# Performance work log

Measured on AMD Instinct MI355X. Metric: run time of the kernel, lower is better.

## Reference

```python
import jax, jax.numpy as jnp
import numpy as np

C_M, C_Z, C = 256, 128, 32
N_SEQ, N_RES = 128, 256


def setup_inputs() -> dict:
    key = jax.random.key(0)
    ks = jax.random.split(key, 8)
    m = jax.random.normal(ks[0], (N_SEQ, N_RES, C_M), dtype=jnp.float32)
    gamma = jnp.ones((C_M,), dtype=jnp.float32)
    beta = jnp.zeros((C_M,), dtype=jnp.float32)
    s = 1.0 / np.sqrt(C_M)
    W1 = jax.random.normal(ks[1], (C_M, C), dtype=jnp.float32) * s
    b1 = jax.random.normal(ks[2], (C,), dtype=jnp.float32) * 0.01
    W2 = jax.random.normal(ks[3], (C_M, C), dtype=jnp.float32) * s
    b2 = jax.random.normal(ks[4], (C,), dtype=jnp.float32) * 0.01
    Wout = jax.random.normal(ks[5], (C * C, C_Z), dtype=jnp.float32) / np.sqrt(C * C)
    bout = jax.random.normal(ks[6], (C_Z,), dtype=jnp.float32) * 0.01
    return {"m": m, "gamma": gamma, "beta": beta, "W1": W1, "b1": b1,
            "W2": W2, "b2": b2, "Wout": Wout, "bout": bout}


def _layernorm(x, gamma, beta, eps=1e-5):
    mu = jnp.mean(x, axis=-1, keepdims=True)
    var = jnp.var(x, axis=-1, keepdims=True)
    return (x - mu) * jax.lax.rsqrt(var + eps) * gamma + beta


def reference(m, gamma, beta, W1, b1, W2, b2, Wout, bout):
    n_seq = m.shape[-3]
    mn = _layernorm(m, gamma, beta)              # (s, i, c_m)
    a = mn @ W1 + b1                              # (s, i, c)
    b = mn @ W2 + b2                              # (s, j, c)
    o = jnp.einsum('sic,sjk->ijck', a, b)        # (i, j, c, c)
    o = o.reshape(o.shape[0], o.shape[1], -1)    # (i, j, c*c)
    z = (o @ Wout + bout) / n_seq                # (i, j, c_z)
    return z
```

## Files before the change

kernel.cpp:

```cpp
#include <hip/hip_runtime.h>
#include <hip/hip_bf16.h>

typedef __attribute__((ext_vector_type(8))) short short8;
typedef __attribute__((ext_vector_type(4))) short short4v;
typedef __attribute__((ext_vector_type(4))) float f32x4;

#define WS_A   0
#define WS_B   (8192 * 128 * 2)
#define WS_WT  (2 * 8192 * 128 * 2)
#define WS_W12 (WS_WT + 128 * 1024 * 2)

static __device__ __forceinline__ short f2bf(float x) {
    __hip_bfloat16 h = __float2bfloat16(x);
    return *reinterpret_cast<short*>(&h);
}

typedef __attribute__((address_space(3))) unsigned int lds_u32;
typedef const __attribute__((address_space(1))) unsigned int glb_u32;
static __device__ __forceinline__ void stage16(const void* g, void* l) {
    __builtin_amdgcn_global_load_lds((glb_u32*)g, (lds_u32*)l, 16, 0, 0);
}

__global__ __launch_bounds__(256) void k_prep(const float* __restrict__ Wout,
                                              const float* __restrict__ W1,
                                              const float* __restrict__ W2,
                                              __hip_bfloat16* __restrict__ WoutT,
                                              __hip_bfloat16* __restrict__ W12bf) {
    int idx = blockIdx.x * 256 + threadIdx.x;
    if (blockIdx.x < 512) {
        int z = idx >> 10, ck = idx & 1023;
        WoutT[idx] = __float2bfloat16(Wout[ck * 128 + z]);
    } else {
        idx -= 512 * 256;
        int c = idx >> 8, d = idx & 255;
        W12bf[idx] = __float2bfloat16(c < 32 ? W1[d * 32 + c] : W2[d * 32 + (c - 32)]);
    }
}

__global__ __launch_bounds__(256) void k_lnproj(const float* __restrict__ mm,
                                                const float* __restrict__ gamma,
                                                const float* __restrict__ beta,
                                                const float* __restrict__ b1,
                                                const float* __restrict__ b2,
                                                const __hip_bfloat16* __restrict__ W12bf,
                                                __hip_bfloat16* __restrict__ Ap,
                                                __hip_bfloat16* __restrict__ Bp) {
    __shared__ char sMN[4][8192];
    __shared__ char sW[32768];
    const int t    = threadIdx.x;
    const int lane = t & 63;
    const int wid  = t >> 6;
    const int gw   = blockIdx.x * 4 + wid;
    const int i_   = gw & 255;
    const int sb   = (gw >> 8) * 16;

    #pragma unroll
    for (int it = 0; it < 8; it++) {
        const int idx = it * 256 + t;
        const int row = idx >> 5;
        const int L   = (idx & 31) * 16;
        *(short8*)(sW + row * 512 + (L ^ ((row & 7) << 4))) =
            *(const short8*)((const short*)W12bf + idx * 8);
    }

    float4 g4  = *(const float4*)&gamma[lane * 4];
    float4 be4 = *(const float4*)&beta[lane * 4];
    char* my = sMN[wid];

    #pragma unroll
    for (int rr = 0; rr < 16; rr++) {
        float4 x = *(const float4*)&mm[((size_t)(sb + rr) * 256 + i_) * 256 + lane * 4];
        float s  = x.x + x.y + x.z + x.w;
        float ss = x.x * x.x + x.y * x.y + x.z * x.z + x.w * x.w;
        #pragma unroll
        for (int off = 32; off; off >>= 1) {
            s  += __shfl_xor(s, off);
            ss += __shfl_xor(ss, off);
        }
        float mu  = s * (1.f / 256.f);
        float var = ss * (1.f / 256.f) - mu * mu;
        float rs  = rsqrtf(var + 1e-5f);
        short4v v;
        v.x = f2bf((x.x - mu) * rs * g4.x + be4.x);
        v.y = f2bf((x.y - mu) * rs * g4.y + be4.y);
        v.z = f2bf((x.z - mu) * rs * g4.z + be4.z);
        v.w = f2bf((x.w - mu) * rs * g4.w + be4.w);
        *(short4v*)(my + rr * 512 + ((lane * 8) ^ ((rr & 7) << 4))) = v;
    }
    __syncthreads();

    const int g = lane >> 4, r16 = lane & 15;

    f32x4 acc[4];
    #pragma unroll
    for (int nf = 0; nf < 4; nf++) {
        int col = nf * 16 + r16;
        float bv = (col < 32) ? b1[col] : b2[col - 32];
        acc[nf] = (f32x4){bv, bv, bv, bv};
    }
    #pragma unroll
    for (int ks = 0; ks < 8; ks++) {
        const int L = ks * 64 + g * 16;
        short8 af = *(const short8*)(my + r16 * 512 + (L ^ ((r16 & 7) << 4)));
        #pragma unroll
        for (int nf = 0; nf < 4; nf++) {
            short8 bfv = *(const short8*)(sW + (nf * 16 + r16) * 512 + (L ^ ((r16 & 7) << 4)));
            acc[nf] = __builtin_amdgcn_mfma_f32_16x16x32_bf16(af, bfv, acc[nf], 0, 0, 0);
        }
    }
    #pragma unroll
    for (int nf = 0; nf < 4; nf++) {
        int col = nf * 16 + r16;
        short* Out = (short*)((col < 32) ? Ap : Bp);
        int cr = col & 31;
        short4v v;
        v.x = f2bf(acc[nf][0]); v.y = f2bf(acc[nf][1]);
        v.z = f2bf(acc[nf][2]); v.w = f2bf(acc[nf][3]);
        *(short4v*)&Out[(i_ * 32 + cr) * 128 + sb + g * 4] = v;
    }
}

extern __shared__ char lds[];

__global__ __launch_bounds__(512, 1) void k_gemm6(const __hip_bfloat16* __restrict__ Apb,
                                                  const __hip_bfloat16* __restrict__ Bpb,
                                                  const __hip_bfloat16* __restrict__ WoutT,
                                                  const float* __restrict__ bout,
                                                  float* __restrict__ out) {
    const int t = threadIdx.x, lane = t & 63, wid = t >> 6;
    const int g = lane >> 4, r16 = lane & 15;
    const int wr = wid >> 2, wc = wid & 3;
    const int bid = (blockIdx.x & 7) * 128 + (blockIdx.x >> 3);
    const int bi = bid >> 5, bj = bid & 31;

    const short* gA = (const short*)Apb + (size_t)bi * 256 * 128;
    const short* gB = (const short*)Bpb + (size_t)bj * 256 * 128;

    const int srow8 = lane >> 3;
    const int sgran = (lane & 7) ^ srow8;
    #pragma unroll
    for (int kh = 0; kh < 2; kh++) {
        #pragma unroll
        for (int rd = 0; rd < 4; rd++) {
            const int row = rd * 64 + wid * 8 + srow8;
            stage16(gB + row * 128 + kh * 64 + sgran * 8,
                    lds + kh * 65536 + rd * 8192 + wid * 1024);
            stage16(gA + row * 128 + kh * 64 + sgran * 8,
                    lds + kh * 65536 + 32768 + rd * 8192 + wid * 1024);
        }
    }

    asm volatile("s_waitcnt vmcnt(8)" ::: "memory");
    __builtin_amdgcn_s_barrier();

    f32x4 acc[8][4];
    #pragma unroll
    for (int mf = 0; mf < 8; mf++)
        #pragma unroll
        for (int nf = 0; nf < 4; nf++)
            acc[mf][nf] = (f32x4){0.f, 0.f, 0.f, 0.f};

    #pragma unroll
    for (int kh = 0; kh < 2; kh++) {
        if (kh) {
            asm volatile("s_waitcnt vmcnt(0)" ::: "memory");
            __builtin_amdgcn_s_barrier();
        }
        const char* sBb = lds + kh * 65536;
        const char* sAb = lds + kh * 65536 + 32768;
        #pragma unroll
        for (int ksl = 0; ksl < 2; ksl++) {
            short8 af[8], bfv[4];
            #pragma unroll
            for (int mf = 0; mf < 8; mf++) {
                const int row = wr * 128 + mf * 16 + r16;
                af[mf] = *(const short8*)(sBb + row * 128 + (((ksl * 4 + g) ^ (row & 7)) << 4));
            }
            #pragma unroll
            for (int nf = 0; nf < 4; nf++) {
                const int row = wc * 64 + nf * 16 + r16;
                bfv[nf] = *(const short8*)(sAb + row * 128 + (((ksl * 4 + g) ^ (row & 7)) << 4));
            }
            __builtin_amdgcn_s_setprio(1);
            #pragma unroll
            for (int mf = 0; mf < 8; mf++)
                #pragma unroll
                for (int nf = 0; nf < 4; nf++)
                    acc[mf][nf] = __builtin_amdgcn_mfma_f32_16x16x32_bf16(af[mf], bfv[nf], acc[mf][nf], 0, 0, 0);
            __builtin_amdgcn_s_setprio(0);
        }
    }
    __builtin_amdgcn_s_barrier();

    const int z = wid * 16 + r16;
    const float bv = bout[z];
    f32x4 acc2[4];
    #pragma unroll
    for (int pf = 0; pf < 4; pf++) acc2[pf] = (f32x4){bv, bv, bv, bv};
    const short* wtz = (const short*)WoutT + z * 1024 + g * 8;

    short8 wA[4], wB[4];

    #define WLOAD(buf, h, grp)                                                           \
        {                                                                                \
            _Pragma("unroll")                                                            \
            for (int q = 0; q < 4; q++)                                                  \
                buf[q] = *(const short8*)&wtz[(h) * 512 + ((grp) * 4 + q) * 32];         \
        }

    #define WCOMP(buf, h, grp)                                                           \
        {                                                                                \
            const char* sPh = lds + (h) * 65536;                                         \
            __builtin_amdgcn_s_setprio(1);                                               \
            _Pragma("unroll")                                                            \
            for (int q = 0; q < 4; q++) {                                                \
                const int L = ((grp) * 4 + q) * 64 + g * 16;                             \
                _Pragma("unroll")                                                        \
                for (int pf = 0; pf < 4; pf++) {                                         \
                    const int row = pf * 16 + r16;                                       \
                    short8 pv = *(const short8*)(sPh + row * 1024 +                      \
                                                 (L ^ ((((L >> 7) ^ row) & 7) << 4)));   \
                    acc2[pf] = __builtin_amdgcn_mfma_f32_16x16x32_bf16(pv, buf[q], acc2[pf], 0, 0, 0); \
                }                                                                        \
            }                                                                            \
            __builtin_amdgcn_s_setprio(0);                                               \
        }

    #define REPACK(h)                                                                    \
        {                                                                                \
            char* sPh = lds + (h) * 65536;                                               \
            _Pragma("unroll")                                                            \
            for (int nq = 0; nq < 2; nq++) {                                             \
                const int nf = (h) + nq * 2;                                             \
                const int p = (wc * 2 + nq) * 8 + wr * 4;                                \
                _Pragma("unroll")                                                        \
                for (int mf = 0; mf < 8; mf++) {                                         \
                    const int pp = p + (mf >> 1);                                        \
                    const int L = r16 * 64 + (mf & 1) * 32 + g * 8;                      \
                    short4v v;                                                           \
                    v.x = f2bf(acc[mf][nf][0]); v.y = f2bf(acc[mf][nf][1]);              \
                    v.z = f2bf(acc[mf][nf][2]); v.w = f2bf(acc[mf][nf][3]);              \
                    *(short4v*)(sPh + pp * 1024 + (L ^ ((((L >> 7) ^ pp) & 7) << 4))) = v; \
                }                                                                        \
            }                                                                            \
        }

    WLOAD(wA, 0, 0)
    WLOAD(wB, 0, 1)
    REPACK(0)
    asm volatile("s_waitcnt lgkmcnt(0)" ::: "memory");
    __builtin_amdgcn_s_barrier();
    REPACK(1)

    WCOMP(wA, 0, 0) WLOAD(wA, 0, 2)
    WCOMP(wB, 0, 1) WLOAD(wB, 0, 3)
    WCOMP(wA, 0, 2) WLOAD(wA, 1, 0)
    WCOMP(wB, 0, 3) WLOAD(wB, 1, 1)

    asm volatile("s_waitcnt lgkmcnt(0)" ::: "memory");
    __builtin_amdgcn_s_barrier();

    WCOMP(wA, 1, 0) WLOAD(wA, 1, 2)
    WCOMP(wB, 1, 1) WLOAD(wB, 1, 3)
    WCOMP(wA, 1, 2)
    WCOMP(wB, 1, 3)

    #pragma unroll
    for (int pf = 0; pf < 4; pf++) {
        #pragma unroll
        for (int reg = 0; reg < 4; reg++) {
            const int p = pf * 16 + g * 4 + reg;
            const int ig = bi * 8 + (p >> 3), jg = bj * 8 + (p & 7);
            out[((size_t)(ig * 256 + jg)) * 128 + z] = acc2[pf][reg] * (1.f / 128.f);
        }
    }
    #undef REPACK
    #undef WLOAD
    #undef WCOMP
}

extern "C" void kernel_launch(void* const* d_in, const int* in_sizes, int n_in,
                              void* d_out, int out_size, void* d_ws, size_t ws_size,
                              hipStream_t stream) {
    const float* mm    = (const float*)d_in[0];
    const float* gamma = (const float*)d_in[1];
    const float* beta  = (const float*)d_in[2];
    const float* W1    = (const float*)d_in[3];
    const float* b1    = (const float*)d_in[4];
    const float* W2    = (const float*)d_in[5];
    const float* b2    = (const float*)d_in[6];
    const float* Wout  = (const float*)d_in[7];
    const float* bout  = (const float*)d_in[8];

    __hip_bfloat16* Ap    = (__hip_bfloat16*)((char*)d_ws + WS_A);
    __hip_bfloat16* Bp    = (__hip_bfloat16*)((char*)d_ws + WS_B);
    __hip_bfloat16* WoutT = (__hip_bfloat16*)((char*)d_ws + WS_WT);
    __hip_bfloat16* W12bf = (__hip_bfloat16*)((char*)d_ws + WS_W12);
    float* out = (float*)d_out;

    (void)hipFuncSetAttribute(reinterpret_cast<const void*>(k_gemm6),
                              hipFuncAttributeMaxDynamicSharedMemorySize, 131072);

    hipLaunchKernelGGL(k_prep, dim3(576), dim3(256), 0, stream, Wout, W1, W2, WoutT, W12bf);
    hipLaunchKernelGGL(k_lnproj, dim3(512), dim3(256), 0, stream,
                       mm, gamma, beta, b1, b2, W12bf, Ap, Bp);
    hipLaunchKernelGGL(k_gemm6, dim3(1024), dim3(512), 131072, stream,
                       Ap, Bp, WoutT, bout, out);
}
```

Before: 71.51 us.

## Retile epilogue GEMM to 32x32 per-wave tiles with rolling Wout prefetch

The epilogue that multiplies the outer-product tile by Wout is re-tiled. Each wave now computes two z-columns by two p-row groups (a 32x32 tile) instead of 16 z by 64 p. This halves the number of LDS reads per MFMA, and each loaded Wout fragment now feeds two MFMAs. Wout fragments are prefetched four steps ahead in a rolling register buffer. The cost is more global Wout traffic per wave, since each wave reads two z rows, and different register pressure.

```diff
diff --git a/kernel.cpp b/kernel.cpp
--- a/kernel.cpp
+++ b/kernel.cpp
@@ -122,11 +122,11 @@
 
 extern __shared__ char lds[];
 
-__global__ __launch_bounds__(512, 1) void k_gemm6(const __hip_bfloat16* __restrict__ Apb,
-                                                  const __hip_bfloat16* __restrict__ Bpb,
-                                                  const __hip_bfloat16* __restrict__ WoutT,
-                                                  const float* __restrict__ bout,
-                                                  float* __restrict__ out) {
+__global__ __launch_bounds__(512, 1) void k_gemm10(const __hip_bfloat16* __restrict__ Apb,
+                                                   const __hip_bfloat16* __restrict__ Bpb,
+                                                   const __hip_bfloat16* __restrict__ WoutT,
+                                                   const float* __restrict__ bout,
+                                                   float* __restrict__ out) {
     const int t = threadIdx.x, lane = t & 63, wid = t >> 6;
     const int g = lane >> 4, r16 = lane & 15;
     const int wr = wid >> 2, wc = wid & 3;
@@ -192,39 +192,21 @@
     }
     __builtin_amdgcn_s_barrier();
 
-    const int z = wid * 16 + r16;
-    const float bv = bout[z];
-    f32x4 acc2[4];
-    #pragma unroll
-    for (int pf = 0; pf < 4; pf++) acc2[pf] = (f32x4){bv, bv, bv, bv};
-    const short* wtz = (const short*)WoutT + z * 1024 + g * 8;
-
-    short8 wA[4], wB[4];
-
-    #define WLOAD(buf, h, grp)                                                           \
-        {                                                                                \
-            _Pragma("unroll")                                                            \
-            for (int q = 0; q < 4; q++)                                                  \
-                buf[q] = *(const short8*)&wtz[(h) * 512 + ((grp) * 4 + q) * 32];         \
-        }
-
-    #define WCOMP(buf, h, grp)                                                           \
-        {                                                                                \
-            const char* sPh = lds + (h) * 65536;                                         \
-            __builtin_amdgcn_s_setprio(1);                                               \
-            _Pragma("unroll")                                                            \
-            for (int q = 0; q < 4; q++) {                                                \
-                const int L = ((grp) * 4 + q) * 64 + g * 16;                             \
-                _Pragma("unroll")                                                        \
-                for (int pf = 0; pf < 4; pf++) {                                         \
-                    const int row = pf * 16 + r16;                                       \
-                    short8 pv = *(const short8*)(sPh + row * 1024 +                      \
-                                                 (L ^ ((((L >> 7) ^ row) & 7) << 4)));   \
-                    acc2[pf] = __builtin_amdgcn_mfma_f32_16x16x32_bf16(pv, buf[q], acc2[pf], 0, 0, 0); \
-                }                                                                        \
-            }                                                                            \
-            __builtin_amdgcn_s_setprio(0);                                               \
-        }
+    const int zgi = wid >> 1, pg = wid & 1;
+    const int z0 = zgi * 32 + r16;
+    const int z1 = zgi * 32 + 16 + r16;
+    const short* wt = (const short*)WoutT;
+    const short* wtz0 = wt + z0 * 1024 + g * 8;
+    const short* wtz1 = wt + z1 * 1024 + g * 8;
+
+    short8 Wr[4][2];
+    #pragma unroll
+    for (int d = 0; d < 4; d++) {
+        Wr[d][0] = *(const short8*)&wtz0[d * 32];
+        Wr[d][1] = *(const short8*)&wtz1[d * 32];
+    }
+    const float bv0 = bout[z0];
+    const float bv1 = bout[z1];
 
     #define REPACK(h)                                                                    \
         {                                                                                \
@@ -245,38 +227,60 @@
             }                                                                            \
         }
 
-    WLOAD(wA, 0, 0)
-    WLOAD(wB, 0, 1)
     REPACK(0)
     asm volatile("s_waitcnt lgkmcnt(0)" ::: "memory");
     __builtin_amdgcn_s_barrier();
     REPACK(1)
 
-    WCOMP(wA, 0, 0) WLOAD(wA, 0, 2)
-    WCOMP(wB, 0, 1) WLOAD(wB, 0, 3)
-    WCOMP(wA, 0, 2) WLOAD(wA, 1, 0)
-    WCOMP(wB, 0, 3) WLOAD(wB, 1, 1)
-
+    f32x4 e00 = (f32x4){bv0, bv0, bv0, bv0};
+    f32x4 e01 = (f32x4){bv1, bv1, bv1, bv1};
+    f32x4 e10 = (f32x4){bv0, bv0, bv0, bv0};
+    f32x4 e11 = (f32x4){bv1, bv1, bv1, bv1};
+
+    const int row0 = pg * 32 + r16;
+    const int row1 = pg * 32 + 16 + r16;
+    const int k0 = (((0 >> 7) ^ row0) & 7), k1 = (((0 >> 7) ^ row1) & 7);
+
+    #define EPISTEP(ksg)                                                                 \
+        {                                                                                \
+            const char* sPh = lds + ((ksg) >> 4) * 65536;                                \
+            const int L = ((ksg) & 15) * 64 + g * 16;                                    \
+            short8 pv0 = *(const short8*)(sPh + row0 * 1024 +                            \
+                                          (L ^ ((((L >> 7) ^ row0) & 7) << 4)));         \
+            short8 pv1 = *(const short8*)(sPh + row1 * 1024 +                            \
+                                          (L ^ ((((L >> 7) ^ row1) & 7) << 4)));         \
+            __builtin_amdgcn_s_setprio(1);                                               \
+            e00 = __builtin_amdgcn_mfma_f32_16x16x32_bf16(pv0, Wr[(ksg) & 3][0], e00, 0, 0, 0); \
+            e01 = __builtin_amdgcn_mfma_f32_16x16x32_bf16(pv0, Wr[(ksg) & 3][1], e01, 0, 0, 0); \
+            e10 = __builtin_amdgcn_mfma_f32_16x16x32_bf16(pv1, Wr[(ksg) & 3][0], e10, 0, 0, 0); \
+            e11 = __builtin_amdgcn_mfma_f32_16x16x32_bf16(pv1, Wr[(ksg) & 3][1], e11, 0, 0, 0); \
+            __builtin_amdgcn_s_setprio(0);                                               \
+            if ((ksg) < 28) {                                                            \
+                Wr[(ksg) & 3][0] = *(const short8*)&wtz0[((ksg) + 4) * 32];              \
+                Wr[(ksg) & 3][1] = *(const short8*)&wtz1[((ksg) + 4) * 32];              \
+            }                                                                            \
+        }
+
+    #pragma unroll
+    for (int ksg = 0; ksg < 16; ksg++) EPISTEP(ksg)
     asm volatile("s_waitcnt lgkmcnt(0)" ::: "memory");
     __builtin_amdgcn_s_barrier();
-
-    WCOMP(wA, 1, 0) WLOAD(wA, 1, 2)
-    WCOMP(wB, 1, 1) WLOAD(wB, 1, 3)
-    WCOMP(wA, 1, 2)
-    WCOMP(wB, 1, 3)
-
-    #pragma unroll
-    for (int pf = 0; pf < 4; pf++) {
-        #pragma unroll
-        for (int reg = 0; reg < 4; reg++) {
-            const int p = pf * 16 + g * 4 + reg;
-            const int ig = bi * 8 + (p >> 3), jg = bj * 8 + (p & 7);
-            out[((size_t)(ig * 256 + jg)) * 128 + z] = acc2[pf][reg] * (1.f / 128.f);
-        }
+    #pragma unroll
+    for (int ksg = 16; ksg < 32; ksg++) EPISTEP(ksg)
+
+    #pragma unroll
+    for (int reg = 0; reg < 4; reg++) {
+        const int p0 = pg * 32 + g * 4 + reg;
+        const int p1 = pg * 32 + 16 + g * 4 + reg;
+        const size_t o0 = ((size_t)((bi * 8 + (p0 >> 3)) * 256 + bj * 8 + (p0 & 7))) * 128;
+        const size_t o1 = ((size_t)((bi * 8 + (p1 >> 3)) * 256 + bj * 8 + (p1 & 7))) * 128;
+        out[o0 + z0] = e00[reg] * (1.f / 128.f);
+        out[o0 + z1] = e01[reg] * (1.f / 128.f);
+        out[o1 + z0] = e10[reg] * (1.f / 128.f);
+        out[o1 + z1] = e11[reg] * (1.f / 128.f);
     }
     #undef REPACK
-    #undef WLOAD
-    #undef WCOMP
+    #undef EPISTEP
 }
 
 extern "C" void kernel_launch(void* const* d_in, const int* in_sizes, int n_in,
@@ -298,12 +302,12 @@
     __hip_bfloat16* W12bf = (__hip_bfloat16*)((char*)d_ws + WS_W12);
     float* out = (float*)d_out;
 
-    (void)hipFuncSetAttribute(reinterpret_cast<const void*>(k_gemm6),
+    (void)hipFuncSetAttribute(reinterpret_cast<const void*>(k_gemm10),
                               hipFuncAttributeMaxDynamicSharedMemorySize, 131072);
 
     hipLaunchKernelGGL(k_prep, dim3(576), dim3(256), 0, stream, Wout, W1, W2, WoutT, W12bf);
     hipLaunchKernelGGL(k_lnproj, dim3(512), dim3(256), 0, stream,
                        mm, gamma, beta, b1, b2, W12bf, Ap, Bp);
-    hipLaunchKernelGGL(k_gemm6, dim3(1024), dim3(512), 131072, stream,
+    hipLaunchKernelGGL(k_gemm10, dim3(1024), dim3(512), 131072, stream,
                        Ap, Bp, WoutT, bout, out);
 }
```

Result: slower. 99.37 us (+39.0%).

## Split fused outer-product/projection kernel into two GEMMs via global bf16 intermediate

Applied to the files above, without the earlier changes.

Splits the fused kernel that computed the outer product and immediately projected it through Wout into two kernels. The first writes the bf16 outer-product tensor (65536 x 1024) to workspace. The second is a separate double-buffered GEMM against WoutT, tuned for two blocks per CU. This trades about 128MB of extra HBM write and read traffic for better occupancy and simpler pipelining in each stage. It falls back to the fused kernel when the workspace is too small.

```diff
diff --git a/kernel.cpp b/kernel.cpp
--- a/kernel.cpp
+++ b/kernel.cpp
@@ -9,6 +9,8 @@
 #define WS_B   (8192 * 128 * 2)
 #define WS_WT  (2 * 8192 * 128 * 2)
 #define WS_W12 (WS_WT + 128 * 1024 * 2)
+#define WS_O   (WS_W12 + 32768)
+#define WS_O_BYTES ((size_t)65536 * 1024 * 2)
 
 static __device__ __forceinline__ short f2bf(float x) {
     __hip_bfloat16 h = __float2bfloat16(x);
@@ -122,11 +124,9 @@
 
 extern __shared__ char lds[];
 
-__global__ __launch_bounds__(512, 1) void k_gemm6(const __hip_bfloat16* __restrict__ Apb,
+__global__ __launch_bounds__(512, 1) void k_gemmA(const __hip_bfloat16* __restrict__ Apb,
                                                   const __hip_bfloat16* __restrict__ Bpb,
-                                                  const __hip_bfloat16* __restrict__ WoutT,
-                                                  const float* __restrict__ bout,
-                                                  float* __restrict__ out) {
+                                                  short* __restrict__ gO) {
     const int t = threadIdx.x, lane = t & 63, wid = t >> 6;
     const int g = lane >> 4, r16 = lane & 15;
     const int wr = wid >> 2, wc = wid & 3;
@@ -190,6 +190,190 @@
             __builtin_amdgcn_s_setprio(0);
         }
     }
+
+    const size_t Rb = ((size_t)bi * 32 + bj) * 64;
+    #pragma unroll
+    for (int nf = 0; nf < 4; nf++) {
+        #pragma unroll
+        for (int mf = 0; mf < 8; mf++) {
+            const int p   = (wc * 2 + (nf >> 1)) * 8 + wr * 4 + (mf >> 1);
+            const int ck0 = ((nf & 1) * 16 + r16) * 32 + (mf & 1) * 16 + g * 4;
+            short4v v;
+            v.x = f2bf(acc[mf][nf][0]); v.y = f2bf(acc[mf][nf][1]);
+            v.z = f2bf(acc[mf][nf][2]); v.w = f2bf(acc[mf][nf][3]);
+            *(short4v*)&gO[(Rb + p) * 1024 + ck0] = v;
+        }
+    }
+}
+
+__global__ __launch_bounds__(512, 2) void k_gemmB(const short* __restrict__ gO,
+                                                  const __hip_bfloat16* __restrict__ WoutT,
+                                                  const float* __restrict__ bout,
+                                                  float* __restrict__ out) {
+    const int t = threadIdx.x, lane = t & 63, wid = t >> 6;
+    const int g = lane >> 4, r16 = lane & 15;
+    const int wr = wid >> 2, wc = wid & 3;
+    const size_t R0 = (size_t)blockIdx.x * 128;
+    const short* wtW = (const short*)WoutT;
+    const int z0 = wc * 32 + r16;
+    const int z1 = wc * 32 + 16 + r16;
+
+    #define STAGEC(c, b)                                                                 \
+        {                                                                                \
+            _Pragma("unroll")                                                            \
+            for (int i = 0; i < 4; i++) {                                                \
+                const int row = i * 32 + wid * 4 + (lane >> 4);                          \
+                const int sg  = lane & 15;                                               \
+                const int ssg = (sg & 8) | ((sg & 7) ^ (row & 7));                       \
+                stage16(gO + (R0 + row) * 1024 + (c) * 128 + ssg * 8,                    \
+                        lds + (b) * 32768 + i * 8192 + wid * 1024);                      \
+            }                                                                            \
+        }
+
+    #define WLOADC(B, c)                                                                 \
+        {                                                                                \
+            _Pragma("unroll")                                                            \
+            for (int ks = 0; ks < 4; ks++) {                                             \
+                B[ks]     = *(const short8*)&wtW[z0 * 1024 + (c) * 128 + ks * 32 + g * 8]; \
+                B[4 + ks] = *(const short8*)&wtW[z1 * 1024 + (c) * 128 + ks * 32 + g * 8]; \
+            }                                                                            \
+        }
+
+    #define COMPC(b, B)                                                                  \
+        {                                                                                \
+            _Pragma("unroll")                                                            \
+            for (int ks = 0; ks < 4; ks++) {                                             \
+                short8 av[4];                                                            \
+                _Pragma("unroll")                                                        \
+                for (int mf = 0; mf < 4; mf++) {                                         \
+                    const int row = wr * 64 + mf * 16 + r16;                             \
+                    const int gr  = ks * 4 + g;                                          \
+                    const int swz = (gr & 8) | ((gr & 7) ^ (row & 7));                   \
+                    av[mf] = *(const short8*)(lds + (b) * 32768 + row * 256 + swz * 16); \
+                }                                                                        \
+                __builtin_amdgcn_s_setprio(1);                                           \
+                _Pragma("unroll")                                                        \
+                for (int mf = 0; mf < 4; mf++) {                                         \
+                    acc[mf][0] = __builtin_amdgcn_mfma_f32_16x16x32_bf16(av[mf], B[ks],     acc[mf][0], 0, 0, 0); \
+                    acc[mf][1] = __builtin_amdgcn_mfma_f32_16x16x32_bf16(av[mf], B[4 + ks], acc[mf][1], 0, 0, 0); \
+                }                                                                        \
+                __builtin_amdgcn_s_setprio(0);                                           \
+            }                                                                            \
+        }
+
+    #define CH(c, b, WC, WN, LAST)                                                       \
+        {                                                                                \
+            if (!(LAST)) { STAGEC((c) + 1, 1 - (b)) WLOADC(WN, (c) + 1) }                \
+            if (LAST) { asm volatile("s_waitcnt vmcnt(0)" ::: "memory"); }               \
+            else      { asm volatile("s_waitcnt vmcnt(12)" ::: "memory"); }              \
+            __builtin_amdgcn_s_barrier();                                                \
+            COMPC(b, WC)                                                                 \
+            __builtin_amdgcn_s_barrier();                                                \
+        }
+
+    short8 W0[8], W1[8];
+    STAGEC(0, 0)
+    WLOADC(W0, 0)
+
+    const float bv0 = bout[z0];
+    const float bv1 = bout[z1];
+    f32x4 acc[4][2];
+    #pragma unroll
+    for (int mf = 0; mf < 4; mf++) {
+        acc[mf][0] = (f32x4){bv0, bv0, bv0, bv0};
+        acc[mf][1] = (f32x4){bv1, bv1, bv1, bv1};
+    }
+
+    CH(0, 0, W0, W1, 0) CH(1, 1, W1, W0, 0) CH(2, 0, W0, W1, 0) CH(3, 1, W1, W0, 0)
+    CH(4, 0, W0, W1, 0) CH(5, 1, W1, W0, 0) CH(6, 0, W0, W1, 0) CH(7, 1, W1, W0, 1)
+
+    #pragma unroll
+    for (int mf = 0; mf < 4; mf++) {
+        #pragma unroll
+        for (int reg = 0; reg < 4; reg++) {
+            const size_t R = R0 + wr * 64 + mf * 16 + g * 4 + reg;
+            const int tile = (int)(R >> 6), p = (int)(R & 63);
+            const int ig = (tile >> 5) * 8 + (p >> 3);
+            const int jg = (tile & 31) * 8 + (p & 7);
+            const size_t ob = ((size_t)(ig * 256 + jg)) * 128;
+            out[ob + z0] = acc[mf][0][reg] * (1.f / 128.f);
+            out[ob + z1] = acc[mf][1][reg] * (1.f / 128.f);
+        }
+    }
+    #undef STAGEC
+    #undef WLOADC
+    #undef COMPC
+    #undef CH
+}
+
+__global__ __launch_bounds__(512, 1) void k_gemm6(const __hip_bfloat16* __restrict__ Apb,
+                                                  const __hip_bfloat16* __restrict__ Bpb,
+                                                  const __hip_bfloat16* __restrict__ WoutT,
+                                                  const float* __restrict__ bout,
+                                                  float* __restrict__ out) {
+    const int t = threadIdx.x, lane = t & 63, wid = t >> 6;
+    const int g = lane >> 4, r16 = lane & 15;
+    const int wr = wid >> 2, wc = wid & 3;
+    const int bid = (blockIdx.x & 7) * 128 + (blockIdx.x >> 3);
+    const int bi = bid >> 5, bj = bid & 31;
+
+    const short* gA = (const short*)Apb + (size_t)bi * 256 * 128;
+    const short* gB = (const short*)Bpb + (size_t)bj * 256 * 128;
+
+    const int srow8 = lane >> 3;
+    const int sgran = (lane & 7) ^ srow8;
+    #pragma unroll
+    for (int kh = 0; kh < 2; kh++) {
+        #pragma unroll
+        for (int rd = 0; rd < 4; rd++) {
+            const int row = rd * 64 + wid * 8 + srow8;
+            stage16(gB + row * 128 + kh * 64 + sgran * 8,
+                    lds + kh * 65536 + rd * 8192 + wid * 1024);
+            stage16(gA + row * 128 + kh * 64 + sgran * 8,
+                    lds + kh * 65536 + 32768 + rd * 8192 + wid * 1024);
+        }
+    }
+
+    asm volatile("s_waitcnt vmcnt(8)" ::: "memory");
+    __builtin_amdgcn_s_barrier();
+
+    f32x4 acc[8][4];
+    #pragma unroll
+    for (int mf = 0; mf < 8; mf++)
+        #pragma unroll
+        for (int nf = 0; nf < 4; nf++)
+            acc[mf][nf] = (f32x4){0.f, 0.f, 0.f, 0.f};
+
+    #pragma unroll
+    for (int kh = 0; kh < 2; kh++) {
+        if (kh) {
+            asm volatile("s_waitcnt vmcnt(0)" ::: "memory");
+            __builtin_amdgcn_s_barrier();
+        }
+        const char* sBb = lds + kh * 65536;
+        const char* sAb = lds + kh * 65536 + 32768;
+        #pragma unroll
+        for (int ksl = 0; ksl < 2; ksl++) {
+            short8 af[8], bfv[4];
+            #pragma unroll
+            for (int mf = 0; mf < 8; mf++) {
+                const int row = wr * 128 + mf * 16 + r16;
+                af[mf] = *(const short8*)(sBb + row * 128 + (((ksl * 4 + g) ^ (row & 7)) << 4));
+            }
+            #pragma unroll
+            for (int nf = 0; nf < 4; nf++) {
+                const int row = wc * 64 + nf * 16 + r16;
+                bfv[nf] = *(const short8*)(sAb + row * 128 + (((ksl * 4 + g) ^ (row & 7)) << 4));
+            }
+            __builtin_amdgcn_s_setprio(1);
+            #pragma unroll
+            for (int mf = 0; mf < 8; mf++)
+                #pragma unroll
+                for (int nf = 0; nf < 4; nf++)
+                    acc[mf][nf] = __builtin_amdgcn_mfma_f32_16x16x32_bf16(af[mf], bfv[nf], acc[mf][nf], 0, 0, 0);
+            __builtin_amdgcn_s_setprio(0);
+        }
+    }
     __builtin_amdgcn_s_barrier();
 
     const int z = wid * 16 + r16;
@@ -207,7 +391,6 @@
             for (int q = 0; q < 4; q++)                                                  \
                 buf[q] = *(const short8*)&wtz[(h) * 512 + ((grp) * 4 + q) * 32];         \
         }
-
     #define WCOMP(buf, h, grp)                                                           \
         {                                                                                \
             const char* sPh = lds + (h) * 65536;                                         \
@@ -225,7 +408,6 @@
             }                                                                            \
             __builtin_amdgcn_s_setprio(0);                                               \
         }
-
     #define REPACK(h)                                                                    \
         {                                                                                \
             char* sPh = lds + (h) * 65536;                                               \
@@ -296,14 +478,27 @@
     __hip_bfloat16* Bp    = (__hip_bfloat16*)((char*)d_ws + WS_B);
     __hip_bfloat16* WoutT = (__hip_bfloat16*)((char*)d_ws + WS_WT);
     __hip_bfloat16* W12bf = (__hip_bfloat16*)((char*)d_ws + WS_W12);
+    short*          gO    = (short*)((char*)d_ws + WS_O);
     float* out = (float*)d_out;
 
+    (void)hipFuncSetAttribute(reinterpret_cast<const void*>(k_gemmA),
+                              hipFuncAttributeMaxDynamicSharedMemorySize, 131072);
+    (void)hipFuncSetAttribute(reinterpret_cast<const void*>(k_gemmB),
+                              hipFuncAttributeMaxDynamicSharedMemorySize, 65536);
     (void)hipFuncSetAttribute(reinterpret_cast<const void*>(k_gemm6),
                               hipFuncAttributeMaxDynamicSharedMemorySize, 131072);
 
     hipLaunchKernelGGL(k_prep, dim3(576), dim3(256), 0, stream, Wout, W1, W2, WoutT, W12bf);
     hipLaunchKernelGGL(k_lnproj, dim3(512), dim3(256), 0, stream,
                        mm, gamma, beta, b1, b2, W12bf, Ap, Bp);
-    hipLaunchKernelGGL(k_gemm6, dim3(1024), dim3(512), 131072, stream,
-                       Ap, Bp, WoutT, bout, out);
-}
+
+    const bool big_ws = (ws_size >= (size_t)WS_O + WS_O_BYTES);
+    if (big_ws) {
+        hipLaunchKernelGGL(k_gemmA, dim3(1024), dim3(512), 131072, stream, Ap, Bp, gO);
+        hipLaunchKernelGGL(k_gemmB, dim3(512), dim3(512), 65536, stream,
+                           gO, WoutT, bout, out);
+    } else {
+        hipLaunchKernelGGL(k_gemm6, dim3(1024), dim3(512), 131072, stream,
+                           Ap, Bp, WoutT, bout, out);
+    }
+}
```

Measured after the change: 110.1 us. +54.0%, slower.

## Halve LDS footprint of fused GEMM by reusing one 64KB buffer

Applied to the files above, without the earlier changes.

The fused outer-product/projection kernel now stages the two K halves into a single 64KB LDS region in sequence instead of loading both into 128KB up front. The repacked intermediate halves also reuse the same region, with extra barriers between phases. Launch bounds change to request 4 blocks per CU so more workgroups can be resident and hide latency. The cost is losing the overlap of the second half's load with compute, plus added barriers. The kernel also still keeps 128 fp32 accumulator registers per thread, which may leave occupancy limited by registers.

```diff
diff --git a/kernel.cpp b/kernel.cpp
--- a/kernel.cpp
+++ b/kernel.cpp
@@ -122,11 +122,11 @@
 
 extern __shared__ char lds[];
 
-__global__ __launch_bounds__(512, 1) void k_gemm6(const __hip_bfloat16* __restrict__ Apb,
-                                                  const __hip_bfloat16* __restrict__ Bpb,
-                                                  const __hip_bfloat16* __restrict__ WoutT,
-                                                  const float* __restrict__ bout,
-                                                  float* __restrict__ out) {
+__global__ __launch_bounds__(512, 4) void k_gemm13(const __hip_bfloat16* __restrict__ Apb,
+                                                   const __hip_bfloat16* __restrict__ Bpb,
+                                                   const __hip_bfloat16* __restrict__ WoutT,
+                                                   const float* __restrict__ bout,
+                                                   float* __restrict__ out) {
     const int t = threadIdx.x, lane = t & 63, wid = t >> 6;
     const int g = lane >> 4, r16 = lane & 15;
     const int wr = wid >> 2, wc = wid & 3;
@@ -138,20 +138,18 @@
 
     const int srow8 = lane >> 3;
     const int sgran = (lane & 7) ^ srow8;
-    #pragma unroll
-    for (int kh = 0; kh < 2; kh++) {
-        #pragma unroll
-        for (int rd = 0; rd < 4; rd++) {
-            const int row = rd * 64 + wid * 8 + srow8;
-            stage16(gB + row * 128 + kh * 64 + sgran * 8,
-                    lds + kh * 65536 + rd * 8192 + wid * 1024);
-            stage16(gA + row * 128 + kh * 64 + sgran * 8,
-                    lds + kh * 65536 + 32768 + rd * 8192 + wid * 1024);
-        }
-    }
-
-    asm volatile("s_waitcnt vmcnt(8)" ::: "memory");
-    __builtin_amdgcn_s_barrier();
+
+    #define STAGEKH(kh)                                                                  \
+        {                                                                                \
+            _Pragma("unroll")                                                            \
+            for (int rd = 0; rd < 4; rd++) {                                             \
+                const int row = rd * 64 + wid * 8 + srow8;                               \
+                stage16(gB + row * 128 + (kh) * 64 + sgran * 8,                          \
+                        lds + rd * 8192 + wid * 1024);                                   \
+                stage16(gA + row * 128 + (kh) * 64 + sgran * 8,                          \
+                        lds + 32768 + rd * 8192 + wid * 1024);                           \
+            }                                                                            \
+        }
 
     f32x4 acc[8][4];
     #pragma unroll
@@ -160,26 +158,25 @@
         for (int nf = 0; nf < 4; nf++)
             acc[mf][nf] = (f32x4){0.f, 0.f, 0.f, 0.f};
 
+    STAGEKH(0)
+    asm volatile("s_waitcnt vmcnt(0)" ::: "memory");
+    __builtin_amdgcn_s_barrier();
+
     #pragma unroll
     for (int kh = 0; kh < 2; kh++) {
-        if (kh) {
-            asm volatile("s_waitcnt vmcnt(0)" ::: "memory");
-            __builtin_amdgcn_s_barrier();
-        }
-        const char* sBb = lds + kh * 65536;
-        const char* sAb = lds + kh * 65536 + 32768;
         #pragma unroll
         for (int ksl = 0; ksl < 2; ksl++) {
             short8 af[8], bfv[4];
             #pragma unroll
             for (int mf = 0; mf < 8; mf++) {
                 const int row = wr * 128 + mf * 16 + r16;
-                af[mf] = *(const short8*)(sBb + row * 128 + (((ksl * 4 + g) ^ (row & 7)) << 4));
+                af[mf] = *(const short8*)(lds + row * 128 + (((ksl * 4 + g) ^ (row & 7)) << 4));
             }
             #pragma unroll
             for (int nf = 0; nf < 4; nf++) {
                 const int row = wc * 64 + nf * 16 + r16;
-                bfv[nf] = *(const short8*)(sAb + row * 128 + (((ksl * 4 + g) ^ (row & 7)) << 4));
+                bfv[nf] = *(const short8*)(lds + 32768 + row * 128 +
+                                           (((ksl * 4 + g) ^ (row & 7)) << 4));
             }
             __builtin_amdgcn_s_setprio(1);
             #pragma unroll
@@ -189,8 +186,14 @@
                     acc[mf][nf] = __builtin_amdgcn_mfma_f32_16x16x32_bf16(af[mf], bfv[nf], acc[mf][nf], 0, 0, 0);
             __builtin_amdgcn_s_setprio(0);
         }
-    }
-    __builtin_amdgcn_s_barrier();
+        asm volatile("s_waitcnt lgkmcnt(0)" ::: "memory");
+        __builtin_amdgcn_s_barrier();
+        if (kh == 0) {
+            STAGEKH(1)
+            asm volatile("s_waitcnt vmcnt(0)" ::: "memory");
+            __builtin_amdgcn_s_barrier();
+        }
+    }
 
     const int z = wid * 16 + r16;
     const float bv = bout[z];
@@ -208,9 +211,8 @@
                 buf[q] = *(const short8*)&wtz[(h) * 512 + ((grp) * 4 + q) * 32];         \
         }
 
-    #define WCOMP(buf, h, grp)                                                           \
+    #define WCOMP(buf, grp)                                                              \
         {                                                                                \
-            const char* sPh = lds + (h) * 65536;                                         \
             __builtin_amdgcn_s_setprio(1);                                               \
             _Pragma("unroll")                                                            \
             for (int q = 0; q < 4; q++) {                                                \
@@ -218,7 +220,7 @@
                 _Pragma("unroll")                                                        \
                 for (int pf = 0; pf < 4; pf++) {                                         \
                     const int row = pf * 16 + r16;                                       \
-                    short8 pv = *(const short8*)(sPh + row * 1024 +                      \
+                    short8 pv = *(const short8*)(lds + row * 1024 +                      \
                                                  (L ^ ((((L >> 7) ^ row) & 7) << 4)));   \
                     acc2[pf] = __builtin_amdgcn_mfma_f32_16x16x32_bf16(pv, buf[q], acc2[pf], 0, 0, 0); \
                 }                                                                        \
@@ -228,7 +230,6 @@
 
     #define REPACK(h)                                                                    \
         {                                                                                \
-            char* sPh = lds + (h) * 65536;                                               \
             _Pragma("unroll")                                                            \
             for (int nq = 0; nq < 2; nq++) {                                             \
                 const int nf = (h) + nq * 2;                                             \
@@ -240,7 +241,7 @@
                     short4v v;                                                           \
                     v.x = f2bf(acc[mf][nf][0]); v.y = f2bf(acc[mf][nf][1]);              \
                     v.z = f2bf(acc[mf][nf][2]); v.w = f2bf(acc[mf][nf][3]);              \
-                    *(short4v*)(sPh + pp * 1024 + (L ^ ((((L >> 7) ^ pp) & 7) << 4))) = v; \
+                    *(short4v*)(lds + pp * 1024 + (L ^ ((((L >> 7) ^ pp) & 7) << 4))) = v; \
                 }                                                                        \
             }                                                                            \
         }
@@ -250,20 +251,22 @@
     REPACK(0)
     asm volatile("s_waitcnt lgkmcnt(0)" ::: "memory");
     __builtin_amdgcn_s_barrier();
-    REPACK(1)
-
-    WCOMP(wA, 0, 0) WLOAD(wA, 0, 2)
-    WCOMP(wB, 0, 1) WLOAD(wB, 0, 3)
-    WCOMP(wA, 0, 2) WLOAD(wA, 1, 0)
-    WCOMP(wB, 0, 3) WLOAD(wB, 1, 1)
+
+    WCOMP(wA, 0) WLOAD(wA, 0, 2)
+    WCOMP(wB, 1) WLOAD(wB, 0, 3)
+    WCOMP(wA, 2) WLOAD(wA, 1, 0)
+    WCOMP(wB, 3) WLOAD(wB, 1, 1)
 
     asm volatile("s_waitcnt lgkmcnt(0)" ::: "memory");
     __builtin_amdgcn_s_barrier();
-
-    WCOMP(wA, 1, 0) WLOAD(wA, 1, 2)
-    WCOMP(wB, 1, 1) WLOAD(wB, 1, 3)
-    WCOMP(wA, 1, 2)
-    WCOMP(wB, 1, 3)
+    REPACK(1)
+    asm volatile("s_waitcnt lgkmcnt(0)" ::: "memory");
+    __builtin_amdgcn_s_barrier();
+
+    WCOMP(wA, 0) WLOAD(wA, 1, 2)
+    WCOMP(wB, 1) WLOAD(wB, 1, 3)
+    WCOMP(wA, 2)
+    WCOMP(wB, 3)
 
     #pragma unroll
     for (int pf = 0; pf < 4; pf++) {
@@ -274,6 +277,7 @@
             out[((size_t)(ig * 256 + jg)) * 128 + z] = acc2[pf][reg] * (1.f / 128.f);
         }
     }
+    #undef STAGEKH
     #undef REPACK
     #undef WLOAD
     #undef WCOMP
@@ -298,12 +302,12 @@
     __hip_bfloat16* W12bf = (__hip_bfloat16*)((char*)d_ws + WS_W12);
     float* out = (float*)d_out;
 
-    (void)hipFuncSetAttribute(reinterpret_cast<const void*>(k_gemm6),
-                              hipFuncAttributeMaxDynamicSharedMemorySize, 131072);
+    (void)hipFuncSetAttribute(reinterpret_cast<const void*>(k_gemm13),
+                              hipFuncAttributeMaxDynamicSharedMemorySize, 65536);
 
     hipLaunchKernelGGL(k_prep, dim3(576), dim3(256), 0, stream, Wout, W1, W2, WoutT, W12bf);
     hipLaunchKernelGGL(k_lnproj, dim3(512), dim3(256), 0, stream,
                        mm, gamma, beta, b1, b2, W12bf, Ap, Bp);
-    hipLaunchKernelGGL(k_gemm6, dim3(1024), dim3(512), 131072, stream,
+    hipLaunchKernelGGL(k_gemm13, dim3(1024), dim3(512), 65536, stream,
                        Ap, Bp, WoutT, bout, out);
 }
```

Measured after the change: 208.2 us. 2.91x slower.
